# Optimization experiments

Measured on AMD Instinct MI355X. Metric: run time of the kernel, lower is better.

The kernel has to match this reference:

```python
import jax, jax.numpy as jnp
import numpy as np

HIDDEN = 2048
NUM_HEADS = 16
HEAD_DIM = HIDDEN // NUM_HEADS
INIT_RANGE = 0.02


def setup_inputs() -> dict:
    key = jax.random.key(0)
    ks = jax.random.split(key, 5)
    B, S = 2, 2048
    hidden_states = jax.random.normal(ks[0], (B, S, HIDDEN), dtype=jnp.float32)
    # Linear weights stored torch-style [out, in]; biases zero-init per _init_weights
    def w(k):
        return INIT_RANGE * jax.random.normal(k, (HIDDEN, HIDDEN), dtype=jnp.float32)
    return {
        "hidden_states": hidden_states,
        "wq": w(ks[1]), "bq": jnp.zeros((HIDDEN,), jnp.float32),
        "wk": w(ks[2]), "bk": jnp.zeros((HIDDEN,), jnp.float32),
        "wv": w(ks[3]), "bv": jnp.zeros((HIDDEN,), jnp.float32),
        "wo": w(ks[4]), "bo": jnp.zeros((HIDDEN,), jnp.float32),
    }


def _split_heads(x):
    # [B,S,H] -> [B,nh,S,hd]
    B, S, _ = x.shape
    return x.reshape(B, S, NUM_HEADS, HEAD_DIM).transpose(0, 2, 1, 3)


def reference(hidden_states, wq, bq, wk, bk, wv, bv, wo, bo):
    B, S, H = hidden_states.shape
    scale = 1.0 / np.sqrt(HEAD_DIM).astype(np.float32)

    q = _split_heads(hidden_states @ wq.T + bq)  # [B,nh,S,hd]
    k = _split_heads(hidden_states @ wk.T + bk)
    v = _split_heads(hidden_states @ wv.T + bv)

    attn = jnp.einsum('bhqd,bhkd->bhqk', q, k) * scale  # [B,nh,S,S]
    # causal mask: -inf above diagonal, 0 on/below
    causal = jnp.where(
        jnp.tril(jnp.ones((S, S), dtype=bool)),
        jnp.float32(0.0), jnp.float32(-jnp.inf))
    attn = attn + causal
    probs = jax.nn.softmax(attn, axis=-1)
    out = jnp.einsum('bhqk,bhkd->bhqd', probs, v)  # [B,nh,S,hd]
    out = out.transpose(0, 2, 1, 3).reshape(B, S, H)  # merge heads
    return out @ wo.T + bo
```

## Files before the change

### kernel.cpp

```cpp
#include <hip/hip_runtime.h>
#include <stdint.h>

typedef unsigned short u16;
typedef __attribute__((ext_vector_type(8))) short short8;
typedef __attribute__((ext_vector_type(4))) short short4v;
typedef __attribute__((ext_vector_type(4))) float float4v;

union V8u { short8 v; short4v h[2]; u16 u[8]; unsigned w[4]; };

__device__ __forceinline__ u16 f2bf(float f) {
  unsigned u = __float_as_uint(f);
  u = u + 0x7FFFu + ((u >> 16) & 1u);
  return (u16)(u >> 16);
}
__device__ __forceinline__ float4v fzero() {
  float4v z = {0.f, 0.f, 0.f, 0.f};
  return z;
}
__device__ __forceinline__ void gl_lds16(const u16* g, u16* l) {
  __builtin_amdgcn_global_load_lds(
      (const __attribute__((address_space(1))) void*)g,
      (__attribute__((address_space(3))) void*)l, 16, 0, 0);
}

#define MFMA16(a, b, c) __builtin_amdgcn_mfma_f32_16x16x32_bf16((a), (b), (c), 0, 0, 0)

__global__ void conv5_f32_bf16(const float* __restrict__ X,
                               const float* __restrict__ w0,
                               const float* __restrict__ w1,
                               const float* __restrict__ w2,
                               u16* __restrict__ dst, long seg) {
  const int y = blockIdx.y;
  const float* s = (y < 2) ? (X + (long)y * seg)
                           : (y == 2 ? w0 : (y == 3 ? w1 : w2));
  u16* d = dst + (long)y * seg;
  const long i = ((long)blockIdx.x * 256 + threadIdx.x) * 8;
  if (i >= seg) return;
  float4 a = *(const float4*)&s[i];
  float4 b = *(const float4*)&s[i + 4];
  V8u o;
  o.u[0] = f2bf(a.x); o.u[1] = f2bf(a.y); o.u[2] = f2bf(a.z); o.u[3] = f2bf(a.w);
  o.u[4] = f2bf(b.x); o.u[5] = f2bf(b.y); o.u[6] = f2bf(b.z); o.u[7] = f2bf(b.w);
  *(short8*)&d[i] = o.v;
}

__global__ void conv_f32_bf16(const float* __restrict__ in, u16* __restrict__ out, long n) {
  const long i = ((long)blockIdx.x * 256 + threadIdx.x) * 8;
  if (i >= n) return;
  float4 a = *(const float4*)&in[i];
  float4 b = *(const float4*)&in[i + 4];
  V8u o;
  o.u[0] = f2bf(a.x); o.u[1] = f2bf(a.y); o.u[2] = f2bf(a.z); o.u[3] = f2bf(a.w);
  o.u[4] = f2bf(b.x); o.u[5] = f2bf(b.y); o.u[6] = f2bf(b.z); o.u[7] = f2bf(b.w);
  *(short8*)&out[i] = o.v;
}

template <bool OUTF32>
__global__ __launch_bounds__(512, 2) void gemm_bal(
    const u16* __restrict__ X, const u16* __restrict__ Wb,
    const float* __restrict__ b0, const float* __restrict__ b1,
    const float* __restrict__ b2, void* __restrict__ Out,
    int K, int cpx)
{
  __shared__ __align__(16) u16 lds[3][3][8192];

  const int t = threadIdx.x;
  const int lane = t & 63;
  const int wave = t >> 6;
  const int quad = lane >> 4, l16 = lane & 15;
  const int wm = wave >> 2, wn = wave & 3;

  const int bid = (int)blockIdx.x;
  const int swz = (bid & 7) * cpx + (bid >> 3);
  const int by = swz & 31;
  const int bx = swz >> 5;
  const long m0 = (long)by * 128;
  const long n0 = (long)bx * 256;

  const u16* pA[2]; const u16* pBl[2]; const u16* pBu[2];
  #pragma unroll
  for (int l = 0; l < 2; ++l) {
    const int d = l * 8192 + t * 16;
    const int o = d ^ ((d >> 3) & 0x70);
    const int r = o >> 7;
    const int c = (o & 127) >> 1;
    pA[l]  = X  + (m0 + r) * (long)K + c;
    pBl[l] = Wb + (n0 + r) * (long)K + c;
    pBu[l] = Wb + (n0 + 128 + r) * (long)K + c;
  }

  int offk[2];
  #pragma unroll
  for (int kk = 0; kk < 2; ++kk)
    offk[kk] = l16 * 128 + ((kk * 64 + quad * 16) ^ ((l16 & 7) << 4));

  float4v acc[4][4];
  #pragma unroll
  for (int i = 0; i < 4; ++i)
    #pragma unroll
    for (int n = 0; n < 4; ++n) acc[i][n] = fzero();

#define STG(buf_, reg_, ptr_, kt_) do {                                        \
    gl_lds16(ptr_[0] + (long)(kt_) * 64, &lds[buf_][reg_][t * 8]);             \
    gl_lds16(ptr_[1] + (long)(kt_) * 64, &lds[buf_][reg_][4096 + t * 8]);      \
  } while (0)

#define BAR() do { asm volatile("s_barrier" ::: "memory");                     \
                   __builtin_amdgcn_sched_barrier(0); } while (0)

  const int NT = K >> 6;

  STG(0, 0, pA, 0);  STG(0, 1, pBl, 0);  STG(0, 2, pBu, 0);
  STG(1, 0, pA, 1);  STG(1, 1, pBl, 1);  STG(1, 2, pBu, 1);
  asm volatile("s_waitcnt vmcnt(6)" ::: "memory");
  BAR();

  int buf = 0, sb = 2;
  for (int kt = 0; kt < NT; ++kt) {
    const int s2 = (kt + 2 < NT) ? kt + 2 : NT - 1;
    const char* Ab = (const char*)&lds[buf][0][0] + wm * 8192;
    const char* Bb = (const char*)&lds[buf][1 + (wn >> 1)][0] + (wn & 1) * 8192;

    short8 a[4][2], b[4][2];

    STG(sb, 0, pA, s2);
    STG(sb, 1, pBl, s2);
    STG(sb, 2, pBu, s2);

    #pragma unroll
    for (int i = 0; i < 4; ++i)
      #pragma unroll
      for (int kk = 0; kk < 2; ++kk)
        a[i][kk] = *(const short8*)(Ab + i * 2048 + offk[kk]);
    #pragma unroll
    for (int n = 0; n < 4; ++n)
      #pragma unroll
      for (int kk = 0; kk < 2; ++kk)
        b[n][kk] = *(const short8*)(Bb + n * 2048 + offk[kk]);

    __builtin_amdgcn_s_setprio(1);
    #pragma unroll
    for (int i = 0; i < 4; ++i)
      #pragma unroll
      for (int n = 0; n < 4; ++n)
        #pragma unroll
        for (int kk = 0; kk < 2; ++kk)
          acc[i][n] = MFMA16(a[i][kk], b[n][kk], acc[i][n]);
    __builtin_amdgcn_s_setprio(0);

    asm volatile("s_waitcnt vmcnt(6)" ::: "memory");
    BAR();

    buf = (buf == 2) ? 0 : buf + 1;
    sb  = (sb  == 2) ? 0 : sb  + 1;
  }
  asm volatile("s_waitcnt vmcnt(0)" ::: "memory");

#undef STG
#undef BAR

  #pragma unroll
  for (int n = 0; n < 4; ++n) {
    const int cg = (int)n0 + wn * 64 + n * 16 + l16;
    const int z = cg >> 11, col = cg & 2047;
    const float* Bp = (z == 0) ? b0 : (z == 1 ? b1 : b2);
    const float bvv = Bp[col];
    #pragma unroll
    for (int i = 0; i < 4; ++i) {
      const long r0 = m0 + wm * 64 + i * 16 + quad * 4;
      #pragma unroll
      for (int r = 0; r < 4; ++r) {
        const long off = (long)z * (4096L * 2048) + (r0 + r) * 2048 + col;
        const float v = acc[i][n][r] + bvv;
        if (OUTF32) ((float*)Out)[off] = v;
        else        ((u16*)Out)[off] = f2bf(v);
      }
    }
  }
}

#define S_LEN 2048
#define HID   2048
#define HD    128

__global__ __launch_bounds__(256, 2) void attn_fwd(
    const u16* __restrict__ Q, const u16* __restrict__ K,
    const u16* __restrict__ V, u16* __restrict__ Ctx)
{
  __shared__ u16 Ks[2][32 * 136];
  __shared__ unsigned Vt[2][128 * 17];
  __shared__ u16 Ps[4 * 2 * 512];

  const int t = threadIdx.x;
  const int lane = t & 63, wave = t >> 6;
  const int quad = lane >> 4, l16 = lane & 15;
  const int b = blockIdx.y >> 4, h = blockIdx.y & 15;

  const long base = (long)b * S_LEN * HID + (long)h * HD;
  const u16* Qp = Q + base;
  const u16* Kp = K + base;
  const u16* Vp = V + base;
  u16* Cp = Ctx + base;

  const int sr2 = t >> 4;
  const int sc8 = (t & 15) * 8;

  short8 onesv;
  {
    V8u ou;
    #pragma unroll
    for (int j = 0; j < 8; ++j) ou.u[j] = 0x3F80;
    onesv = ou.v;
  }
  const float SC = 0.08838834764831845f * 1.4426950408889634f;

  for (int pass = 0; pass < 2; ++pass) {
    const int qb = (pass ? (int)blockIdx.x : 15 - (int)blockIdx.x) * 128;
    const int wqb = qb + wave * 32;

    short8 qf[2][4];
    #pragma unroll
    for (int g = 0; g < 2; ++g) {
      const long qr = wqb + g * 16 + l16;
      #pragma unroll
      for (int kk = 0; kk < 4; ++kk)
        qf[g][kk] = *(const short8*)&Qp[qr * HID + kk * 32 + quad * 8];
    }

    float4v o[2][9];
    #pragma unroll
    for (int g = 0; g < 2; ++g)
      #pragma unroll
      for (int i = 0; i < 9; ++i) o[g][i] = fzero();

    short8 kr0, kr1, vv0, vv1;
    {
      const long g = (long)(2 * sr2) * HID + sc8;
      kr0 = *(const short8*)&Kp[g];
      kr1 = *(const short8*)&Kp[g + HID];
      vv0 = *(const short8*)&Vp[g];
      vv1 = *(const short8*)&Vp[g + HID];
    }
    {
      *(short8*)&Ks[0][(2 * sr2) * 136 + sc8]     = kr0;
      *(short8*)&Ks[0][(2 * sr2 + 1) * 136 + sc8] = kr1;
      V8u a, c; a.v = vv0; c.v = vv1;
      #pragma unroll
      for (int j = 0; j < 8; ++j)
        Vt[0][(sc8 + j) * 17 + sr2] = (unsigned)a.u[j] | ((unsigned)c.u[j] << 16);
    }
    __syncthreads();

    const int T = (qb + 128) >> 5;
    for (int ti = 0; ti < T; ++ti) {
      const int kv0 = ti << 5;
      const int p = ti & 1;

      const bool more = (ti + 1 < T);
      if (more) {
        const long g = (long)(kv0 + 32 + 2 * sr2) * HID + sc8;
        kr0 = *(const short8*)&Kp[g];
        kr1 = *(const short8*)&Kp[g + HID];
        vv0 = *(const short8*)&Vp[g];
        vv1 = *(const short8*)&Vp[g + HID];
      }

      if (kv0 <= wqb) {
        float4v s[2][2];
        #pragma unroll
        for (int g = 0; g < 2; ++g) { s[g][0] = fzero(); s[g][1] = fzero(); }
        #pragma unroll
        for (int ni = 0; ni < 2; ++ni)
          #pragma unroll
          for (int kk = 0; kk < 4; ++kk) {
            short8 kf = *(const short8*)&Ks[p][(ni * 16 + l16) * 136 + kk * 32 + quad * 8];
            s[0][ni] = MFMA16(qf[0][kk], kf, s[0][ni]);
            s[1][ni] = MFMA16(qf[1][kk], kf, s[1][ni]);
          }

        const int pb = wave * 1024;
        #pragma unroll
        for (int g = 0; g < 2; ++g) {
          const int qrow0 = wqb + g * 16 + quad * 4;
          #pragma unroll
          for (int r = 0; r < 4; ++r) {
            float s0 = fminf(s[g][0][r] * SC, 80.f);
            float s1 = fminf(s[g][1][r] * SC, 80.f);
            if (kv0 + l16 > qrow0 + r)      s0 = -1e30f;
            if (kv0 + 16 + l16 > qrow0 + r) s1 = -1e30f;
            Ps[pb + g * 512 + (quad * 4 + r) * 32 + l16]      = f2bf(__builtin_amdgcn_exp2f(s0));
            Ps[pb + g * 512 + (quad * 4 + r) * 32 + 16 + l16] = f2bf(__builtin_amdgcn_exp2f(s1));
          }
        }
        __threadfence_block();
        short8 pf0 = *(const short8*)&Ps[pb + l16 * 32 + quad * 8];
        short8 pf1 = *(const short8*)&Ps[pb + 512 + l16 * 32 + quad * 8];

        #pragma unroll
        for (int dt = 0; dt < 8; ++dt) {
          const unsigned* vp = &Vt[p][(dt * 16 + l16) * 17 + quad * 4];
          V8u vf;
          vf.w[0] = vp[0]; vf.w[1] = vp[1]; vf.w[2] = vp[2]; vf.w[3] = vp[3];
          o[0][dt] = MFMA16(pf0, vf.v, o[0][dt]);
          o[1][dt] = MFMA16(pf1, vf.v, o[1][dt]);
        }
        o[0][8] = MFMA16(pf0, onesv, o[0][8]);
        o[1][8] = MFMA16(pf1, onesv, o[1][8]);
      }

      if (more) {
        *(short8*)&Ks[1 - p][(2 * sr2) * 136 + sc8]     = kr0;
        *(short8*)&Ks[1 - p][(2 * sr2 + 1) * 136 + sc8] = kr1;
        V8u a, c; a.v = vv0; c.v = vv1;
        #pragma unroll
        for (int j = 0; j < 8; ++j)
          Vt[1 - p][(sc8 + j) * 17 + sr2] = (unsigned)a.u[j] | ((unsigned)c.u[j] << 16);
      }
      __syncthreads();
    }

    #pragma unroll
    for (int g = 0; g < 2; ++g)
      #pragma unroll
      for (int r = 0; r < 4; ++r) {
        const float inv = 1.0f / o[g][8][r];
        const long qr = wqb + g * 16 + quad * 4 + r;
        #pragma unroll
        for (int dt = 0; dt < 8; ++dt)
          Cp[qr * HID + dt * 16 + l16] = f2bf(o[g][dt][r] * inv);
      }
  }
}

extern "C" void kernel_launch(void* const* d_in, const int* in_sizes, int n_in,
                              void* d_out, int out_size, void* d_ws, size_t ws_size,
                              hipStream_t stream) {
  const float* X  = (const float*)d_in[0];
  const float* wq = (const float*)d_in[1];
  const float* bq = (const float*)d_in[2];
  const float* wk = (const float*)d_in[3];
  const float* bk = (const float*)d_in[4];
  const float* wv = (const float*)d_in[5];
  const float* bv = (const float*)d_in[6];
  const float* wo = (const float*)d_in[7];
  const float* bo = (const float*)d_in[8];
  float* out = (float*)d_out;

  const long HSZ = 4096L * 2048;
  const long WSZ = 2048L * 2048;
  u16* Qw = (u16*)d_ws;
  u16* Kw = Qw + HSZ;
  u16* Vw = Kw + HSZ;
  u16* Xb = Vw + HSZ;
  u16* Wb = Xb + HSZ;
  u16* W0 = Wb;

  dim3 blk(256);
  conv5_f32_bf16<<<dim3((int)(WSZ / 2048), 5), blk, 0, stream>>>(X, wq, wk, wv, Xb, WSZ);

  gemm_bal<false><<<dim3(768), dim3(512), 0, stream>>>(
      Xb, Wb, bq, bk, bv, Qw, 2048, 96);

  attn_fwd<<<dim3(8, 32), blk, 0, stream>>>(Qw, Kw, Vw, Qw);

  conv_f32_bf16<<<(int)(WSZ / 2048), blk, 0, stream>>>(wo, W0, WSZ);
  gemm_bal<true><<<dim3(256), dim3(512), 0, stream>>>(
      Qw, W0, bo, bo, bo, out, 2048, 32);
}
```

Baseline: 391.2 us.

## Widen QKV GEMM tile to 128x384 and double-buffer with interleaved LDS reads

The GEMM kernel is templated on the number of 64-column B slabs. The fused QKV projection now uses 128x384 tiles over 512 blocks instead of 128x256 over 768, which raises A-tile reuse. The LDS pipeline goes from triple to double buffering with a full vmcnt(0) wait each iteration. LDS fragment reads are split and interleaved between MFMA groups using sched barriers to hide read latency. The trade-off is more accumulator registers and a shallower prefetch depth, which can expose global-load latency.

```diff
diff --git a/kernel.cpp b/kernel.cpp
--- a/kernel.cpp
+++ b/kernel.cpp
@@ -55,14 +55,15 @@
   *(short8*)&out[i] = o.v;
 }
 
-template <bool OUTF32>
+template <int NREP, bool OUTF32>
 __global__ __launch_bounds__(512, 2) void gemm_bal(
     const u16* __restrict__ X, const u16* __restrict__ Wb,
     const float* __restrict__ b0, const float* __restrict__ b1,
     const float* __restrict__ b2, void* __restrict__ Out,
     int K, int cpx)
 {
-  __shared__ __align__(16) u16 lds[3][3][8192];
+  constexpr int NH = NREP / 2;
+  __shared__ __align__(16) u16 lds[2][(2 + NREP) * 4096];
 
   const int t = threadIdx.x;
   const int lane = t & 63;
@@ -75,18 +76,21 @@
   const int by = swz & 31;
   const int bx = swz >> 5;
   const long m0 = (long)by * 128;
-  const long n0 = (long)bx * 256;
-
-  const u16* pA[2]; const u16* pBl[2]; const u16* pBu[2];
+  const long n0 = (long)bx * (64 * NREP);
+
+  const u16* pA[2];
   #pragma unroll
   for (int l = 0; l < 2; ++l) {
     const int d = l * 8192 + t * 16;
     const int o = d ^ ((d >> 3) & 0x70);
-    const int r = o >> 7;
-    const int c = (o & 127) >> 1;
-    pA[l]  = X  + (m0 + r) * (long)K + c;
-    pBl[l] = Wb + (n0 + r) * (long)K + c;
-    pBu[l] = Wb + (n0 + 128 + r) * (long)K + c;
+    pA[l] = X + (m0 + (o >> 7)) * (long)K + ((o & 127) >> 1);
+  }
+  const u16* pB[NREP];
+  #pragma unroll
+  for (int s = 0; s < NREP; ++s) {
+    const int d = s * 8192 + t * 16;
+    const int o = d ^ ((d >> 3) & 0x70);
+    pB[s] = Wb + (n0 + (o >> 7)) * (long)K + ((o & 127) >> 1);
   }
 
   int offk[2];
@@ -94,74 +98,109 @@
   for (int kk = 0; kk < 2; ++kk)
     offk[kk] = l16 * 128 + ((kk * 64 + quad * 16) ^ ((l16 & 7) << 4));
 
-  float4v acc[4][4];
+  float4v acc[4][NREP];
   #pragma unroll
   for (int i = 0; i < 4; ++i)
     #pragma unroll
-    for (int n = 0; n < 4; ++n) acc[i][n] = fzero();
-
-#define STG(buf_, reg_, ptr_, kt_) do {                                        \
-    gl_lds16(ptr_[0] + (long)(kt_) * 64, &lds[buf_][reg_][t * 8]);             \
-    gl_lds16(ptr_[1] + (long)(kt_) * 64, &lds[buf_][reg_][4096 + t * 8]);      \
-  } while (0)
-
-#define BAR() do { asm volatile("s_barrier" ::: "memory");                     \
-                   __builtin_amdgcn_sched_barrier(0); } while (0)
+    for (int j = 0; j < NREP; ++j) acc[i][j] = fzero();
+
+  auto STAGE = [&](u16* Lb, int kt_) {
+    #pragma unroll
+    for (int l = 0; l < 2; ++l)
+      gl_lds16(pA[l] + (long)kt_ * 64, Lb + l * 4096 + t * 8);
+    #pragma unroll
+    for (int s = 0; s < NREP; ++s)
+      gl_lds16(pB[s] + (long)kt_ * 64, Lb + 8192 + s * 4096 + t * 8);
+  };
+
+#define SB() __builtin_amdgcn_sched_barrier(0)
+#define BAR() do { asm volatile("s_barrier" ::: "memory"); SB(); } while (0)
 
   const int NT = K >> 6;
 
-  STG(0, 0, pA, 0);  STG(0, 1, pBl, 0);  STG(0, 2, pBu, 0);
-  STG(1, 0, pA, 1);  STG(1, 1, pBl, 1);  STG(1, 2, pBu, 1);
-  asm volatile("s_waitcnt vmcnt(6)" ::: "memory");
+  STAGE(&lds[0][0], 0);
+  asm volatile("s_waitcnt vmcnt(0)" ::: "memory");
   BAR();
 
-  int buf = 0, sb = 2;
   for (int kt = 0; kt < NT; ++kt) {
-    const int s2 = (kt + 2 < NT) ? kt + 2 : NT - 1;
-    const char* Ab = (const char*)&lds[buf][0][0] + wm * 8192;
-    const char* Bb = (const char*)&lds[buf][1 + (wn >> 1)][0] + (wn & 1) * 8192;
-
-    short8 a[4][2], b[4][2];
-
-    STG(sb, 0, pA, s2);
-    STG(sb, 1, pBl, s2);
-    STG(sb, 2, pBu, s2);
-
-    #pragma unroll
-    for (int i = 0; i < 4; ++i)
-      #pragma unroll
-      for (int kk = 0; kk < 2; ++kk)
-        a[i][kk] = *(const short8*)(Ab + i * 2048 + offk[kk]);
-    #pragma unroll
-    for (int n = 0; n < 4; ++n)
-      #pragma unroll
-      for (int kk = 0; kk < 2; ++kk)
-        b[n][kk] = *(const short8*)(Bb + n * 2048 + offk[kk]);
+    const int buf = kt & 1;
+    const int nkt = (kt + 1 < NT) ? kt + 1 : NT - 1;
+    const char* Ab = (const char*)&lds[buf][0] + wm * 8192;
+    const char* Bb = (const char*)&lds[buf][8192] + wn * (16 * NREP) * 128;
+
+    short8 a[4][2], b[NREP][2];
+
+    STAGE(&lds[buf ^ 1][0], nkt);
+
+    #pragma unroll
+    for (int i = 0; i < 4; ++i)
+      a[i][0] = *(const short8*)(Ab + i * 2048 + offk[0]);
+    #pragma unroll
+    for (int j = 0; j < NH; ++j)
+      b[j][0] = *(const short8*)(Bb + j * 2048 + offk[0]);
+    #pragma unroll
+    for (int j = NH; j < NREP; ++j)
+      b[j][0] = *(const short8*)(Bb + j * 2048 + offk[0]);
+    #pragma unroll
+    for (int i = 0; i < 4; ++i)
+      a[i][1] = *(const short8*)(Ab + i * 2048 + offk[1]);
+    SB();
 
     __builtin_amdgcn_s_setprio(1);
     #pragma unroll
     for (int i = 0; i < 4; ++i)
       #pragma unroll
-      for (int n = 0; n < 4; ++n)
-        #pragma unroll
-        for (int kk = 0; kk < 2; ++kk)
-          acc[i][n] = MFMA16(a[i][kk], b[n][kk], acc[i][n]);
+      for (int j = 0; j < NH; ++j)
+        acc[i][j] = MFMA16(a[i][0], b[j][0], acc[i][j]);
     __builtin_amdgcn_s_setprio(0);
-
-    asm volatile("s_waitcnt vmcnt(6)" ::: "memory");
+    SB();
+
+    #pragma unroll
+    for (int j = 0; j < NH; ++j)
+      b[j][1] = *(const short8*)(Bb + j * 2048 + offk[1]);
+    SB();
+
+    __builtin_amdgcn_s_setprio(1);
+    #pragma unroll
+    for (int i = 0; i < 4; ++i)
+      #pragma unroll
+      for (int j = NH; j < NREP; ++j)
+        acc[i][j] = MFMA16(a[i][0], b[j][0], acc[i][j]);
+    __builtin_amdgcn_s_setprio(0);
+    SB();
+
+    #pragma unroll
+    for (int j = NH; j < NREP; ++j)
+      b[j][1] = *(const short8*)(Bb + j * 2048 + offk[1]);
+    SB();
+
+    __builtin_amdgcn_s_setprio(1);
+    #pragma unroll
+    for (int i = 0; i < 4; ++i)
+      #pragma unroll
+      for (int j = 0; j < NH; ++j)
+        acc[i][j] = MFMA16(a[i][1], b[j][1], acc[i][j]);
+    __builtin_amdgcn_s_setprio(0);
+    SB();
+
+    __builtin_amdgcn_s_setprio(1);
+    #pragma unroll
+    for (int i = 0; i < 4; ++i)
+      #pragma unroll
+      for (int j = NH; j < NREP; ++j)
+        acc[i][j] = MFMA16(a[i][1], b[j][1], acc[i][j]);
+    __builtin_amdgcn_s_setprio(0);
+
+    asm volatile("s_waitcnt vmcnt(0)" ::: "memory");
     BAR();
-
-    buf = (buf == 2) ? 0 : buf + 1;
-    sb  = (sb  == 2) ? 0 : sb  + 1;
-  }
-  asm volatile("s_waitcnt vmcnt(0)" ::: "memory");
-
-#undef STG
+  }
+
+#undef SB
 #undef BAR
 
   #pragma unroll
-  for (int n = 0; n < 4; ++n) {
-    const int cg = (int)n0 + wn * 64 + n * 16 + l16;
+  for (int j = 0; j < NREP; ++j) {
+    const int cg = (int)n0 + wn * (16 * NREP) + j * 16 + l16;
     const int z = cg >> 11, col = cg & 2047;
     const float* Bp = (z == 0) ? b0 : (z == 1 ? b1 : b2);
     const float bvv = Bp[col];
@@ -171,7 +210,7 @@
       #pragma unroll
       for (int r = 0; r < 4; ++r) {
         const long off = (long)z * (4096L * 2048) + (r0 + r) * 2048 + col;
-        const float v = acc[i][n][r] + bvv;
+        const float v = acc[i][j][r] + bvv;
         if (OUTF32) ((float*)Out)[off] = v;
         else        ((u16*)Out)[off] = f2bf(v);
       }
@@ -358,12 +397,12 @@
   dim3 blk(256);
   conv5_f32_bf16<<<dim3((int)(WSZ / 2048), 5), blk, 0, stream>>>(X, wq, wk, wv, Xb, WSZ);
 
-  gemm_bal<false><<<dim3(768), dim3(512), 0, stream>>>(
-      Xb, Wb, bq, bk, bv, Qw, 2048, 96);
+  gemm_bal<6, false><<<dim3(512), dim3(512), 0, stream>>>(
+      Xb, Wb, bq, bk, bv, Qw, 2048, 64);
 
   attn_fwd<<<dim3(8, 32), blk, 0, stream>>>(Qw, Kw, Vw, Qw);
 
   conv_f32_bf16<<<(int)(WSZ / 2048), blk, 0, stream>>>(wo, W0, WSZ);
-  gemm_bal<true><<<dim3(256), dim3(512), 0, stream>>>(
+  gemm_bal<4, true><<<dim3(256), dim3(512), 0, stream>>>(
       Qw, W0, bo, bo, bo, out, 2048, 32);
 }
```

Measured after the change: 391.3 us. Within noise of the previous version (+0.0%).
